# Performance work log

Hardware: AMD Instinct MI355X
Metric: run time of the kernel (lower is better)

## Reference

```python
import jax, jax.numpy as jnp
import numpy as np

D_MODEL = 1024
HEADS = 16
DK = D_MODEL // HEADS  # 64
B, S = 1, 4096


def setup_inputs() -> dict:
    key = jax.random.key(0)
    ks = jax.random.split(key, 11)
    sd = 1.0 / np.sqrt(D_MODEL)
    return {
        "q": jax.random.normal(ks[0], (B, S, D_MODEL), jnp.float32),
        "k": jax.random.normal(ks[1], (B, S, D_MODEL), jnp.float32),
        "v": jax.random.normal(ks[2], (B, S, D_MODEL), jnp.float32),
        "Wq": jax.random.uniform(ks[3], (D_MODEL, D_MODEL), jnp.float32, -sd, sd),
        "bq": jax.random.uniform(ks[4], (D_MODEL,), jnp.float32, -sd, sd),
        "Wk": jax.random.uniform(ks[5], (D_MODEL, DK), jnp.float32, -sd, sd),
        "bk": jax.random.uniform(ks[6], (DK,), jnp.float32, -sd, sd),
        "Wv": jax.random.uniform(ks[7], (D_MODEL, DK), jnp.float32, -sd, sd),
        "bv": jax.random.uniform(ks[8], (DK,), jnp.float32, -sd, sd),
        "Wo": jax.random.uniform(ks[9], (D_MODEL, D_MODEL), jnp.float32, -sd, sd),
        "bo": jax.random.uniform(ks[10], (D_MODEL,), jnp.float32, -sd, sd),
    }


def reference(q, k, v, Wq, bq, Wk, bk, Wv, bv, Wo, bo):
    b, s, d = q.shape
    # projections: q -> [b, H, s, dk]; k, v -> single shared head [b, s, dk]
    qp = (q @ Wq + bq).reshape(b, s, HEADS, DK).transpose(0, 2, 1, 3)
    kp = k @ Wk + bk  # [b, s, dk]
    vp = v @ Wv + bv  # [b, s, dk]
    # NOTE: original module never applies self.scale or dropout — faithful.
    scores = jnp.einsum('bhqd,bkd->bhqk', qp, kp)  # [b, H, s, s]
    attn = jax.nn.softmax(scores, axis=-1)
    out = jnp.einsum('bhqk,bkd->bhqd', attn, vp)  # [b, H, s, dk]
    out = out.transpose(0, 2, 1, 3).reshape(b, s, d)
    return out @ Wo + bo
```

## Files before the change

### kernel.cpp

```cpp
#include <hip/hip_runtime.h>
#include <hip/hip_bf16.h>
#include <stdint.h>

typedef __bf16 bf16_t;
typedef __attribute__((ext_vector_type(8))) __bf16 bf16x8;
typedef __attribute__((ext_vector_type(4))) __bf16 bf16x4;
typedef __attribute__((ext_vector_type(4))) float f32x4;

#define S_LEN 4096
#define DMODEL 1024
#define NHEADS 16
#define DKH 64

__device__ __forceinline__ f32x4 mfma16(bf16x8 a, bf16x8 b, f32x4 c) {
  return __builtin_amdgcn_mfma_f32_16x16x32_bf16(a, b, c, 0, 0, 0);
}

template <typename TS>
__device__ __forceinline__ bf16x8 load8_bf16(const TS* g) {
  bf16x8 o;
  if constexpr (sizeof(TS) == 4) {
    const float4 f0 = *(const float4*)(g);
    const float4 f1 = *(const float4*)(g + 4);
    o[0] = (bf16_t)f0.x; o[1] = (bf16_t)f0.y; o[2] = (bf16_t)f0.z; o[3] = (bf16_t)f0.w;
    o[4] = (bf16_t)f1.x; o[5] = (bf16_t)f1.y; o[6] = (bf16_t)f1.z; o[7] = (bf16_t)f1.w;
  } else {
    o = *(const bf16x8*)(g);
  }
  return o;
}

template <typename TS>
__device__ __forceinline__ void stage_tile64(const TS* __restrict__ g, int gstride,
                                             bf16_t* lds, int rows, int tid) {
  for (int i = tid; i < rows * 8; i += 256) {
    const int row = i >> 3, j = i & 7;
    const int c = j ^ (row & 7);
    bf16x8 v = load8_bf16(g + (size_t)row * gstride + j * 8);
    *(bf16x8*)((char*)lds + row * 128 + c * 16) = v;
  }
}

__device__ __forceinline__ bf16x8 frag64(const bf16_t* lds, int row, int g) {
  return *(const bf16x8*)((const char*)lds + row * 128 + ((g ^ (row & 7)) * 16));
}

__device__ __forceinline__ void gload16(const bf16_t* g, bf16_t* lds) {
  __builtin_amdgcn_global_load_lds(
      (const __attribute__((address_space(1))) unsigned int*)g,
      (__attribute__((address_space(3))) unsigned int*)lds, 16, 0, 0);
}

__global__ __launch_bounds__(256) void convert_bf16(const float* __restrict__ src,
                                                    bf16_t* __restrict__ dst) {
  const size_t i = (size_t)(blockIdx.x * 256 + threadIdx.x) * 8;
  bf16x8 v = load8_bf16(src + i);
  *(bf16x8*)(dst + i) = v;
}

__global__ __launch_bounds__(256) void prep_weights(const float* __restrict__ Wq,
                                                    const float* __restrict__ Wo,
                                                    const float* __restrict__ Wk,
                                                    const float* __restrict__ Wv,
                                                    bf16_t* __restrict__ Wqt,
                                                    bf16_t* __restrict__ Wot,
                                                    bf16_t* __restrict__ Wkt,
                                                    bf16_t* __restrict__ Wvt) {
  const int b = blockIdx.x;
  const float* src; bf16_t* dst; int ss, ds_, bx, by;
  if (b < 256)      { src = Wq; dst = Wqt; ss = 1024; ds_ = 1024; bx = b & 15;         by = b >> 4; }
  else if (b < 512) { src = Wo; dst = Wot; ss = 1024; ds_ = 1024; bx = (b - 256) & 15; by = (b - 256) >> 4; }
  else if (b < 528) { src = Wk; dst = Wkt; ss = 64;   ds_ = 1024; bx = 0;              by = b - 512; }
  else              { src = Wv; dst = Wvt; ss = 64;   ds_ = 1024; bx = 0;              by = b - 528; }

  __shared__ bf16_t t[64][65];
  const int tid = threadIdx.x;
  const int r0 = by * 64, c0 = bx * 64;
#pragma unroll
  for (int it = 0; it < 2; ++it) {
    int idx = tid + it * 256;
    int r = idx >> 3, c8 = idx & 7;
    bf16x8 v = load8_bf16(src + (size_t)(r0 + r) * ss + c0 + c8 * 8);
#pragma unroll
    for (int j = 0; j < 8; ++j) t[c8 * 8 + j][r] = v[j];
  }
  __syncthreads();
#pragma unroll
  for (int it = 0; it < 2; ++it) {
    int idx = tid + it * 256;
    int r = idx >> 3, c8 = idx & 7;
    bf16x8 v;
#pragma unroll
    for (int j = 0; j < 8; ++j) v[j] = t[r][c8 * 8 + j];
    *(bf16x8*)(dst + (size_t)(c0 + r) * ds_ + r0 + c8 * 8) = v;
  }
}

template <typename TC>
__global__ __launch_bounds__(256) void gemm_nt_dma(const bf16_t* __restrict__ A, int lda,
                                                   const bf16_t* __restrict__ Bt, int ldb,
                                                   const float* __restrict__ bias,
                                                   TC* __restrict__ C, int ldc, int K) {
  constexpr int BM = 128, BN = 64;
  __shared__ __align__(16) bf16_t As[2][BM * 64];
  __shared__ __align__(16) bf16_t Bs[2][BN * 64];
  const int tid = threadIdx.x, l = tid & 63, w = tid >> 6;
  const int lr = l & 15, quad = l >> 4;
  const int m0 = blockIdx.y * BM, n0 = blockIdx.x * BN;
  const int wm = w * 32;

  const int srow = l >> 3;
  const int sch = (l & 7) ^ srow;
  const bf16_t* a0 = A + (size_t)(m0 + w * 32 + srow) * lda + sch * 8;
  const bf16_t* b0 = Bt + (size_t)(n0 + w * 16 + srow) * ldb + sch * 8;

  f32x4 zero = {0.f, 0.f, 0.f, 0.f};
  f32x4 acc[2][4];
#pragma unroll
  for (int i = 0; i < 2; ++i)
#pragma unroll
    for (int j = 0; j < 4; ++j) acc[i][j] = zero;

  const int nt = K >> 6;

#pragma unroll
  for (int sub = 0; sub < 4; ++sub)
    gload16(a0 + (size_t)sub * 8 * lda, &As[0][(w * 32 + sub * 8) * 64]);
#pragma unroll
  for (int sub = 0; sub < 2; ++sub)
    gload16(b0 + (size_t)sub * 8 * ldb, &Bs[0][(w * 16 + sub * 8) * 64]);
  asm volatile("s_waitcnt vmcnt(0)" ::: "memory");
  __builtin_amdgcn_s_barrier();
  asm volatile("" ::: "memory");

  for (int t = 0; t < nt; ++t) {
    const int cur = t & 1;
    if (t + 1 < nt) {
#pragma unroll
      for (int sub = 0; sub < 4; ++sub)
        gload16(a0 + (size_t)(t + 1) * 64 + (size_t)sub * 8 * lda,
                &As[cur ^ 1][(w * 32 + sub * 8) * 64]);
#pragma unroll
      for (int sub = 0; sub < 2; ++sub)
        gload16(b0 + (size_t)(t + 1) * 64 + (size_t)sub * 8 * ldb,
                &Bs[cur ^ 1][(w * 16 + sub * 8) * 64]);
    }
    const bf16_t* Ac = &As[cur][0];
    const bf16_t* Bc = &Bs[cur][0];
#pragma unroll
    for (int kc = 0; kc < 2; ++kc) {
      bf16x8 af[2], bfr[4];
#pragma unroll
      for (int rt = 0; rt < 2; ++rt) af[rt] = frag64(Ac, wm + rt * 16 + lr, kc * 4 + quad);
#pragma unroll
      for (int ct = 0; ct < 4; ++ct) bfr[ct] = frag64(Bc, ct * 16 + lr, kc * 4 + quad);
#pragma unroll
      for (int rt = 0; rt < 2; ++rt)
#pragma unroll
        for (int ct = 0; ct < 4; ++ct) acc[rt][ct] = mfma16(af[rt], bfr[ct], acc[rt][ct]);
    }
    asm volatile("s_waitcnt vmcnt(0) lgkmcnt(0)" ::: "memory");
    __builtin_amdgcn_s_barrier();
    asm volatile("" ::: "memory");
  }

#pragma unroll
  for (int rt = 0; rt < 2; ++rt)
#pragma unroll
    for (int ct = 0; ct < 4; ++ct) {
      const int n = n0 + ct * 16 + lr;
      const float bv = bias[n];
      const int mb = m0 + wm + rt * 16 + quad * 4;
#pragma unroll
      for (int r = 0; r < 4; ++r)
        C[(size_t)(mb + r) * ldc + n] = (TC)(acc[rt][ct][r] + bv);
    }
}

template <int KSPLIT>
__global__ __launch_bounds__(256) void gemm_projkv_partial(const float* __restrict__ Ak,
                                                           const float* __restrict__ Av,
                                                           const bf16_t* __restrict__ Wkt,
                                                           const bf16_t* __restrict__ Wvt,
                                                           float* __restrict__ Pk,
                                                           float* __restrict__ Pv) {
  const float* A = blockIdx.z ? Av : Ak;
  const bf16_t* Bt = blockIdx.z ? Wvt : Wkt;
  float* part = blockIdx.z ? Pv : Pk;

  __shared__ __align__(16) bf16_t As[128 * 64];
  __shared__ __align__(16) bf16_t Bs[64 * 64];
  const int tid = threadIdx.x, l = tid & 63, w = tid >> 6;
  const int lr = l & 15, quad = l >> 4;
  const int kp = blockIdx.x, m0 = blockIdx.y * 128;
  const int kBase = kp * (DMODEL / KSPLIT);
  const int wm = w * 32;

  f32x4 zero = {0.f, 0.f, 0.f, 0.f};
  f32x4 acc[2][4];
#pragma unroll
  for (int i = 0; i < 2; ++i)
#pragma unroll
    for (int j = 0; j < 4; ++j) acc[i][j] = zero;

  for (int t = 0; t < (DMODEL / KSPLIT) / 64; ++t) {
    __syncthreads();
    stage_tile64(A + (size_t)m0 * DMODEL + kBase + t * 64, DMODEL, As, 128, tid);
    stage_tile64(Bt + kBase + t * 64, DMODEL, Bs, 64, tid);
    __syncthreads();
#pragma unroll
    for (int kc = 0; kc < 2; ++kc) {
      bf16x8 af[2], bfr[4];
#pragma unroll
      for (int rt = 0; rt < 2; ++rt) af[rt] = frag64(As, wm + rt * 16 + lr, kc * 4 + quad);
#pragma unroll
      for (int ct = 0; ct < 4; ++ct) bfr[ct] = frag64(Bs, ct * 16 + lr, kc * 4 + quad);
#pragma unroll
      for (int rt = 0; rt < 2; ++rt)
#pragma unroll
        for (int ct = 0; ct < 4; ++ct) acc[rt][ct] = mfma16(af[rt], bfr[ct], acc[rt][ct]);
    }
  }
#pragma unroll
  for (int rt = 0; rt < 2; ++rt)
#pragma unroll
    for (int ct = 0; ct < 4; ++ct) {
      const int n = ct * 16 + lr;
      const int mb = m0 + wm + rt * 16 + quad * 4;
#pragma unroll
      for (int r = 0; r < 4; ++r)
        part[(size_t)kp * S_LEN * 64 + (size_t)(mb + r) * 64 + n] = acc[rt][ct][r];
    }
}

__global__ __launch_bounds__(256) void reduce_kv(const float* __restrict__ Pk,
                                                 const float* __restrict__ Pv,
                                                 const float* __restrict__ bk,
                                                 const float* __restrict__ bv,
                                                 bf16_t* __restrict__ kvb,
                                                 bf16_t* __restrict__ vtb) {
  const int gid = blockIdx.x * 256 + threadIdx.x;
  const int s = gid >> 6, d = gid & 63;
  float sk = bk[d], sv = bv[d];
#pragma unroll
  for (int p = 0; p < 8; ++p) {
    sk += Pk[(size_t)p * S_LEN * 64 + gid];
    sv += Pv[(size_t)p * S_LEN * 64 + gid];
  }
  kvb[(size_t)s * 128 + d] = (bf16_t)sk;
  kvb[(size_t)s * 128 + 64 + d] = (bf16_t)sv;
  vtb[(size_t)d * S_LEN + s] = (bf16_t)sv;
}

__global__ __launch_bounds__(512, 4) void mqa_attn(const bf16_t* __restrict__ qp,
                                                   const bf16_t* __restrict__ kvb,
                                                   const bf16_t* __restrict__ vtb,
                                                   bf16_t* __restrict__ outp) {
  __shared__ __align__(16) char smem[49152];
  bf16_t* Ks = (bf16_t*)smem;
  bf16_t* Vs = (bf16_t*)(smem + 16384);
  char*   Ps = smem + 32768;

  const int tid = threadIdx.x, l = tid & 63, w = tid >> 6;
  const int lr = l & 15, quad = l >> 4;
  const int wq = w >> 1, wk = w & 1;
  const int h = blockIdx.y;
  const int q0 = blockIdx.x * 128;
  const int qrA = q0 + wq * 32 + lr;
  const int qrB = qrA + 16;
  char* Pw = Ps + w * 2048;

  const int srow = w * 8 + (l >> 3);
  const int schunk = (l & 7) ^ (srow & 7);
  const bf16_t* ksrc = kvb + (size_t)srow * 128 + schunk * 8;
  const bf16_t* vsrc = vtb + (size_t)srow * S_LEN + schunk * 8;

  const bf16_t* qbA = qp + (size_t)qrA * DMODEL + h * DKH;
  const bf16x8 qfA0 = *(const bf16x8*)(qbA + quad * 8);
  const bf16x8 qfA1 = *(const bf16x8*)(qbA + 32 + quad * 8);
  const bf16_t* qbB = qp + (size_t)qrB * DMODEL + h * DKH;
  const bf16x8 qfB0 = *(const bf16x8*)(qbB + quad * 8);
  const bf16x8 qfB1 = *(const bf16x8*)(qbB + 32 + quad * 8);

  f32x4 zero = {0.f, 0.f, 0.f, 0.f};
  f32x4 o[4][2];
#pragma unroll
  for (int dt = 0; dt < 4; ++dt) { o[dt][0] = zero; o[dt][1] = zero; }
  float liA = 0.f, liB = 0.f;

  gload16(ksrc, Ks + w * 512);
  gload16(vsrc, Vs + w * 512);
  asm volatile("s_waitcnt vmcnt(0)" ::: "memory");
  __builtin_amdgcn_s_barrier();
  asm volatile("" ::: "memory");

  for (int t = 0; t < S_LEN / 64; ++t) {
    const int cur = t & 1;
    if (t + 1 < S_LEN / 64) {
      gload16(ksrc + (size_t)(t + 1) * 8192, Ks + (cur ^ 1) * 4096 + w * 512);
      gload16(vsrc + (size_t)(t + 1) * 64, Vs + (cur ^ 1) * 4096 + w * 512);
    }
    const bf16_t* Kc = Ks + cur * 4096;
    const bf16_t* Vc = Vs + cur * 4096;

    f32x4 st[2][2];
#pragma unroll
    for (int kt = 0; kt < 2; ++kt) {
      const int krow = wk * 32 + kt * 16 + lr;
      const bf16x8 kf0 = frag64(Kc, krow, quad);
      const bf16x8 kf1 = frag64(Kc, krow, 4 + quad);
      f32x4 a0 = mfma16(kf0, qfA0, zero);
      a0 = mfma16(kf1, qfA1, a0);
      st[kt][0] = a0;
      f32x4 a1 = mfma16(kf0, qfB0, zero);
      a1 = mfma16(kf1, qfB1, a1);
      st[kt][1] = a1;
    }

#pragma unroll
    for (int kt = 0; kt < 2; ++kt)
#pragma unroll
      for (int qt = 0; qt < 2; ++qt) {
        bf16x4 pk;
        float rs = 0.f;
#pragma unroll
        for (int r = 0; r < 4; ++r) {
          const float p = __expf(st[kt][qt][r]);
          rs += p;
          pk[r] = (bf16_t)p;
        }
        if (qt == 0) liA += rs; else liB += rs;
        *(bf16x4*)(Pw + lr * 128 +
                   ((((qt << 2) + (kt << 1) + (quad >> 1)) ^ (lr & 7)) << 4) +
                   ((quad & 1) << 3)) = pk;
      }
    asm volatile("s_waitcnt lgkmcnt(0)" ::: "memory");

    const bf16x8 pf0 = *(const bf16x8*)(Pw + lr * 128 + ((quad ^ (lr & 7)) << 4));
    const bf16x8 pf1 = *(const bf16x8*)(Pw + lr * 128 + (((4 + quad) ^ (lr & 7)) << 4));
#pragma unroll
    for (int dt = 0; dt < 4; ++dt) {
      const bf16x8 vf = frag64(Vc, dt * 16 + lr, wk * 4 + quad);
      o[dt][0] = mfma16(vf, pf0, o[dt][0]);
      o[dt][1] = mfma16(vf, pf1, o[dt][1]);
    }

    asm volatile("s_waitcnt vmcnt(0) lgkmcnt(0)" ::: "memory");
    __builtin_amdgcn_s_barrier();
    asm volatile("" ::: "memory");
  }

  liA += __shfl_xor(liA, 16, 64);
  liA += __shfl_xor(liA, 32, 64);
  liB += __shfl_xor(liB, 16, 64);
  liB += __shfl_xor(liB, 32, 64);

  float* liBuf = (float*)Ps;
  if (quad == 0) {
    liBuf[w * 32 + lr] = liA;
    liBuf[w * 32 + 16 + lr] = liB;
  }
  float* Obuf = (float*)smem;
  if (wk == 1) {
#pragma unroll
    for (int dt = 0; dt < 4; ++dt)
#pragma unroll
      for (int qt = 0; qt < 2; ++qt)
        *(f32x4*)(&Obuf[wq * 2048 + (qt * 16 + lr) * 64 + dt * 16 + quad * 4]) = o[dt][qt];
  }
  __syncthreads();
  if (wk == 0) {
    const float ltA = liA + liBuf[(w ^ 1) * 32 + lr];
    const float ltB = liB + liBuf[(w ^ 1) * 32 + 16 + lr];
    const float invA = 1.f / ltA;
    const float invB = 1.f / ltB;
#pragma unroll
    for (int dt = 0; dt < 4; ++dt) {
      const f32x4 pA = *(const f32x4*)(&Obuf[wq * 2048 + lr * 64 + dt * 16 + quad * 4]);
      const f32x4 pB = *(const f32x4*)(&Obuf[wq * 2048 + (16 + lr) * 64 + dt * 16 + quad * 4]);
      bf16x4 ovA, ovB;
#pragma unroll
      for (int rg = 0; rg < 4; ++rg) {
        ovA[rg] = (bf16_t)((o[dt][0][rg] + pA[rg]) * invA);
        ovB[rg] = (bf16_t)((o[dt][1][rg] + pB[rg]) * invB);
      }
      *(bf16x4*)(outp + (size_t)qrA * DMODEL + h * DKH + dt * 16 + quad * 4) = ovA;
      *(bf16x4*)(outp + (size_t)qrB * DMODEL + h * DKH + dt * 16 + quad * 4) = ovB;
    }
  }
}

extern "C" void kernel_launch(void* const* d_in, const int* in_sizes, int n_in,
                              void* d_out, int out_size, void* d_ws, size_t ws_size,
                              hipStream_t stream) {
  const float* q  = (const float*)d_in[0];
  const float* k  = (const float*)d_in[1];
  const float* v  = (const float*)d_in[2];
  const float* Wq = (const float*)d_in[3];
  const float* bq = (const float*)d_in[4];
  const float* Wk = (const float*)d_in[5];
  const float* bk = (const float*)d_in[6];
  const float* Wv = (const float*)d_in[7];
  const float* bv = (const float*)d_in[8];
  const float* Wo = (const float*)d_in[9];
  const float* bo = (const float*)d_in[10];
  float* out = (float*)d_out;
  char* ws = (char*)d_ws;

  const size_t MB = 1u << 20;
  bf16_t* Wqt = (bf16_t*)(ws);
  bf16_t* Wot = (bf16_t*)(ws + 2 * MB);
  bf16_t* Wkt = (bf16_t*)(ws + 4 * MB);
  bf16_t* Wvt = (bf16_t*)(ws + 4 * MB + 131072);
  bf16_t* kvb = (bf16_t*)(ws + 4 * MB + 524288);
  bf16_t* vtb = (bf16_t*)(ws + 5 * MB + 524288);
  float*  Pk   = (float*)(ws + 6 * MB);
  float*  Pv   = (float*)(ws + 14 * MB);
  bf16_t* qb   = (bf16_t*)(ws + 6 * MB);
  bf16_t* qp   = (bf16_t*)(ws + 14 * MB);
  bf16_t* attn = (bf16_t*)(ws + 6 * MB);

  dim3 B(256);
  prep_weights<<<dim3(544), B, 0, stream>>>(Wq, Wo, Wk, Wv, Wqt, Wot, Wkt, Wvt);

  gemm_projkv_partial<8><<<dim3(8, 32, 2), B, 0, stream>>>(k, v, Wkt, Wvt, Pk, Pv);
  reduce_kv<<<dim3(1024), B, 0, stream>>>(Pk, Pv, bk, bv, kvb, vtb);

  convert_bf16<<<dim3(2048), B, 0, stream>>>(q, qb);
  gemm_nt_dma<bf16_t><<<dim3(16, 32), B, 0, stream>>>(qb, 1024, Wqt, 1024, bq, qp, 1024, 1024);

  mqa_attn<<<dim3(32, 16), dim3(512), 0, stream>>>(qp, kvb, vtb, attn);

  gemm_nt_dma<float><<<dim3(16, 32), B, 0, stream>>>(attn, 1024, Wot, 1024, bo, out, 1024, 1024);
}
```

Measured before the change: 244.9 us.

## Double attention KV tile to 128 keys and fold log2e into Q projection

The attention kernel now stages 128 keys per iteration instead of 64. The loop runs half as many times, so there are fewer barriers and waits per key processed. It uses a new 256-byte-row swizzled layout for V^T and an inner two-step loop over 64-key halves. Separately, the Q projection GEMM epilogue multiplies by log2(e) so the softmax can use exp2f instead of __expf. The cost is LDS growing from 48KB to 80KB per block, which may reduce occupancy versus the launch bound of 4 blocks.

```diff
diff --git a/kernel.cpp b/kernel.cpp
--- a/kernel.cpp
+++ b/kernel.cpp
@@ -43,6 +43,11 @@
 
 __device__ __forceinline__ bf16x8 frag64(const bf16_t* lds, int row, int g) {
   return *(const bf16x8*)((const char*)lds + row * 128 + ((g ^ (row & 7)) * 16));
+}
+
+__device__ __forceinline__ bf16x8 frag128(const bf16_t* lds, int row, int c) {
+  const int phys = (c & 8) | ((c ^ (row & 7)) & 7);
+  return *(const bf16x8*)((const char*)lds + row * 256 + phys * 16);
 }
 
 __device__ __forceinline__ void gload16(const bf16_t* g, bf16_t* lds) {
@@ -100,7 +105,8 @@
 __global__ __launch_bounds__(256) void gemm_nt_dma(const bf16_t* __restrict__ A, int lda,
                                                    const bf16_t* __restrict__ Bt, int ldb,
                                                    const float* __restrict__ bias,
-                                                   TC* __restrict__ C, int ldc, int K) {
+                                                   TC* __restrict__ C, int ldc, int K,
+                                                   float escale) {
   constexpr int BM = 128, BN = 64;
   __shared__ __align__(16) bf16_t As[2][BM * 64];
   __shared__ __align__(16) bf16_t Bs[2][BN * 64];
@@ -173,7 +179,7 @@
       const int mb = m0 + wm + rt * 16 + quad * 4;
 #pragma unroll
       for (int r = 0; r < 4; ++r)
-        C[(size_t)(mb + r) * ldc + n] = (TC)(acc[rt][ct][r] + bv);
+        C[(size_t)(mb + r) * ldc + n] = (TC)((acc[rt][ct][r] + bv) * escale);
     }
 }
 
@@ -256,10 +262,10 @@
                                                    const bf16_t* __restrict__ kvb,
                                                    const bf16_t* __restrict__ vtb,
                                                    bf16_t* __restrict__ outp) {
-  __shared__ __align__(16) char smem[49152];
+  __shared__ __align__(16) char smem[81920];
   bf16_t* Ks = (bf16_t*)smem;
-  bf16_t* Vs = (bf16_t*)(smem + 16384);
-  char*   Ps = smem + 32768;
+  bf16_t* Vs = (bf16_t*)(smem + 32768);
+  char*   Ps = smem + 65536;
 
   const int tid = threadIdx.x, l = tid & 63, w = tid >> 6;
   const int lr = l & 15, quad = l >> 4;
@@ -270,10 +276,17 @@
   const int qrB = qrA + 16;
   char* Pw = Ps + w * 2048;
 
-  const int srow = w * 8 + (l >> 3);
-  const int schunk = (l & 7) ^ (srow & 7);
-  const bf16_t* ksrc = kvb + (size_t)srow * 128 + schunk * 8;
-  const bf16_t* vsrc = vtb + (size_t)srow * S_LEN + schunk * 8;
+  const int kr = w * 16 + (l >> 3);
+  const int kch = (l & 7) ^ (kr & 7);
+  const bf16_t* ksrc = kvb + (size_t)kr * 128 + kch * 8;
+
+  const int vp = l & 15;
+  const int vr1 = w * 8 + (l >> 4);
+  const int vr2 = vr1 + 4;
+  const int vg1 = (vp & 8) | ((vp ^ (vr1 & 7)) & 7);
+  const int vg2 = (vp & 8) | ((vp ^ (vr2 & 7)) & 7);
+  const bf16_t* vsrc1 = vtb + (size_t)vr1 * S_LEN + vg1 * 8;
+  const bf16_t* vsrc2 = vtb + (size_t)vr2 * S_LEN + vg2 * 8;
 
   const bf16_t* qbA = qp + (size_t)qrA * DMODEL + h * DKH;
   const bf16x8 qfA0 = *(const bf16x8*)(qbA + quad * 8);
@@ -288,61 +301,71 @@
   for (int dt = 0; dt < 4; ++dt) { o[dt][0] = zero; o[dt][1] = zero; }
   float liA = 0.f, liB = 0.f;
 
-  gload16(ksrc, Ks + w * 512);
-  gload16(vsrc, Vs + w * 512);
+  gload16(ksrc, Ks + w * 1024);
+  gload16(ksrc + 1024, Ks + w * 1024 + 512);
+  gload16(vsrc1, Vs + w * 1024);
+  gload16(vsrc2, Vs + w * 1024 + 512);
   asm volatile("s_waitcnt vmcnt(0)" ::: "memory");
   __builtin_amdgcn_s_barrier();
   asm volatile("" ::: "memory");
 
-  for (int t = 0; t < S_LEN / 64; ++t) {
+  for (int t = 0; t < S_LEN / 128; ++t) {
     const int cur = t & 1;
-    if (t + 1 < S_LEN / 64) {
-      gload16(ksrc + (size_t)(t + 1) * 8192, Ks + (cur ^ 1) * 4096 + w * 512);
-      gload16(vsrc + (size_t)(t + 1) * 64, Vs + (cur ^ 1) * 4096 + w * 512);
-    }
-    const bf16_t* Kc = Ks + cur * 4096;
-    const bf16_t* Vc = Vs + cur * 4096;
-
-    f32x4 st[2][2];
-#pragma unroll
-    for (int kt = 0; kt < 2; ++kt) {
-      const int krow = wk * 32 + kt * 16 + lr;
-      const bf16x8 kf0 = frag64(Kc, krow, quad);
-      const bf16x8 kf1 = frag64(Kc, krow, 4 + quad);
-      f32x4 a0 = mfma16(kf0, qfA0, zero);
-      a0 = mfma16(kf1, qfA1, a0);
-      st[kt][0] = a0;
-      f32x4 a1 = mfma16(kf0, qfB0, zero);
-      a1 = mfma16(kf1, qfB1, a1);
-      st[kt][1] = a1;
-    }
-
-#pragma unroll
-    for (int kt = 0; kt < 2; ++kt)
-#pragma unroll
-      for (int qt = 0; qt < 2; ++qt) {
-        bf16x4 pk;
-        float rs = 0.f;
-#pragma unroll
-        for (int r = 0; r < 4; ++r) {
-          const float p = __expf(st[kt][qt][r]);
-          rs += p;
-          pk[r] = (bf16_t)p;
+    if (t + 1 < S_LEN / 128) {
+      const bf16_t* kn = ksrc + (size_t)(t + 1) * 16384;
+      gload16(kn, Ks + (cur ^ 1) * 8192 + w * 1024);
+      gload16(kn + 1024, Ks + (cur ^ 1) * 8192 + w * 1024 + 512);
+      gload16(vsrc1 + (size_t)(t + 1) * 128, Vs + (cur ^ 1) * 8192 + w * 1024);
+      gload16(vsrc2 + (size_t)(t + 1) * 128, Vs + (cur ^ 1) * 8192 + w * 1024 + 512);
+    }
+    const bf16_t* Kc = Ks + cur * 8192;
+    const bf16_t* Vc = Vs + cur * 8192;
+
+#pragma unroll
+    for (int kk = 0; kk < 2; ++kk) {
+      f32x4 st[2][2];
+#pragma unroll
+      for (int kt = 0; kt < 2; ++kt) {
+        const int krow = wk * 64 + kk * 32 + kt * 16 + lr;
+        const bf16x8 kf0 = frag64(Kc, krow, quad);
+        const bf16x8 kf1 = frag64(Kc, krow, 4 + quad);
+        f32x4 a0 = mfma16(kf0, qfA0, zero);
+        a0 = mfma16(kf1, qfA1, a0);
+        st[kt][0] = a0;
+        f32x4 a1 = mfma16(kf0, qfB0, zero);
+        a1 = mfma16(kf1, qfB1, a1);
+        st[kt][1] = a1;
+      }
+
+      if (kk) asm volatile("s_waitcnt lgkmcnt(0)" ::: "memory");
+
+#pragma unroll
+      for (int kt = 0; kt < 2; ++kt)
+#pragma unroll
+        for (int qt = 0; qt < 2; ++qt) {
+          bf16x4 pk;
+          float rs = 0.f;
+#pragma unroll
+          for (int r = 0; r < 4; ++r) {
+            const float p = exp2f(st[kt][qt][r]);
+            rs += p;
+            pk[r] = (bf16_t)p;
+          }
+          if (qt == 0) liA += rs; else liB += rs;
+          *(bf16x4*)(Pw + lr * 128 +
+                     ((((qt << 2) + (kt << 1) + (quad >> 1)) ^ (lr & 7)) << 4) +
+                     ((quad & 1) << 3)) = pk;
         }
-        if (qt == 0) liA += rs; else liB += rs;
-        *(bf16x4*)(Pw + lr * 128 +
-                   ((((qt << 2) + (kt << 1) + (quad >> 1)) ^ (lr & 7)) << 4) +
-                   ((quad & 1) << 3)) = pk;
+      asm volatile("s_waitcnt lgkmcnt(0)" ::: "memory");
+
+      const bf16x8 pf0 = *(const bf16x8*)(Pw + lr * 128 + ((quad ^ (lr & 7)) << 4));
+      const bf16x8 pf1 = *(const bf16x8*)(Pw + lr * 128 + (((4 + quad) ^ (lr & 7)) << 4));
+#pragma unroll
+      for (int dt = 0; dt < 4; ++dt) {
+        const bf16x8 vf = frag128(Vc, dt * 16 + lr, wk * 8 + kk * 4 + quad);
+        o[dt][0] = mfma16(vf, pf0, o[dt][0]);
+        o[dt][1] = mfma16(vf, pf1, o[dt][1]);
       }
-    asm volatile("s_waitcnt lgkmcnt(0)" ::: "memory");
-
-    const bf16x8 pf0 = *(const bf16x8*)(Pw + lr * 128 + ((quad ^ (lr & 7)) << 4));
-    const bf16x8 pf1 = *(const bf16x8*)(Pw + lr * 128 + (((4 + quad) ^ (lr & 7)) << 4));
-#pragma unroll
-    for (int dt = 0; dt < 4; ++dt) {
-      const bf16x8 vf = frag64(Vc, dt * 16 + lr, wk * 4 + quad);
-      o[dt][0] = mfma16(vf, pf0, o[dt][0]);
-      o[dt][1] = mfma16(vf, pf1, o[dt][1]);
     }
 
     asm volatile("s_waitcnt vmcnt(0) lgkmcnt(0)" ::: "memory");
@@ -427,9 +450,11 @@
   reduce_kv<<<dim3(1024), B, 0, stream>>>(Pk, Pv, bk, bv, kvb, vtb);
 
   convert_bf16<<<dim3(2048), B, 0, stream>>>(q, qb);
-  gemm_nt_dma<bf16_t><<<dim3(16, 32), B, 0, stream>>>(qb, 1024, Wqt, 1024, bq, qp, 1024, 1024);
+  gemm_nt_dma<bf16_t><<<dim3(16, 32), B, 0, stream>>>(qb, 1024, Wqt, 1024, bq, qp, 1024, 1024,
+                                                      1.44269504088896340736f);
 
   mqa_attn<<<dim3(32, 16), dim3(512), 0, stream>>>(qp, kvb, vtb, attn);
 
-  gemm_nt_dma<float><<<dim3(16, 32), B, 0, stream>>>(attn, 1024, Wot, 1024, bo, out, 1024, 1024);
-}
+  gemm_nt_dma<float><<<dim3(16, 32), B, 0, stream>>>(attn, 1024, Wot, 1024, bo, out, 1024, 1024,
+                                                     1.0f);
+}
```

After: 261.5 us. 1.07x slower.
